# Performance work log

Hardware: AMD Instinct MI355X
Metric: run time of the kernel (lower is better)

Reference implementation:

```python
import jax, jax.numpy as jnp
import numpy as np

T, N, D = 512, 32, 1024
H, P, L = 1024, 1024, 4
STDV = 1.0 / np.sqrt(H)


def setup_inputs() -> dict:
    key = jax.random.key(0)
    ks = jax.random.split(key, 11)
    u = lambda k, shape: jax.random.uniform(k, shape, jnp.float32, -STDV, STDV)
    return {
        "x": jax.random.normal(ks[0], (T, N, D), jnp.float32),
        "h0": jax.random.normal(ks[1], (L, N, P), jnp.float32),
        "c0": jax.random.normal(ks[2], (L, N, H), jnp.float32),
        "w_ih": u(ks[3], (L, D, 4 * H)),
        "w_hh": u(ks[4], (L, P, 4 * H)),
        "b_ih": u(ks[5], (L, 4 * H)),
        "b_hh": u(ks[6], (L, 4 * H)),
        "w_ic": u(ks[7], (L, H)),
        "w_fc": u(ks[8], (L, H)),
        "w_oc": u(ks[9], (L, H)),
        "w_hm": u(ks[10], (L, H, P)),
    }


def _run_layer(x, h0, c0, wih, whh, b, wic, wfc, woc, whm):
    # x: (T, N, Din); h0: (N, P); c0: (N, H)
    def step(carry, xt):
        h, c = carry
        a = xt @ wih + h @ whh + b  # (N, 4H)
        ai, af, ag, ao = jnp.split(a, 4, axis=1)
        i = jax.nn.sigmoid(ai + c * wic)
        f = jax.nn.sigmoid(af + c * wfc)
        g = jnp.tanh(ag)
        nc = f * c + i * g
        o = jax.nn.sigmoid(ao + nc * woc)
        nh = (o * jnp.tanh(nc)) @ whm  # projection -> (N, P)
        return (nh, nc), nh

    (hT, cT), ys = jax.lax.scan(step, (h0, c0), x)
    return ys, hT, cT


def reference(x, h0, c0, w_ih, w_hh, b_ih, b_hh, w_ic, w_fc, w_oc, w_hm):
    layer_input = x
    hs, cs = [], []
    for l in range(L):
        b = b_ih[l] + b_hh[l]
        layer_input, hT, cT = _run_layer(
            layer_input, h0[l], c0[l], w_ih[l], w_hh[l], b,
            w_ic[l], w_fc[l], w_oc[l], w_hm[l])
        hs.append(hT)
        cs.append(cT)
    return layer_input, jnp.stack(hs, 0), jnp.stack(cs, 0)
```

## Files before the change

### kernel.cpp

```cpp
#include <hip/hip_runtime.h>
#include <hip/hip_bf16.h>
#include <cstdint>
#include <cstddef>


#define TT 512
#define NBATCH 32
#define HID 1024
#define G4 4096
#define KCAT 2048

typedef __attribute__((ext_vector_type(4))) float f32x4;
typedef __attribute__((ext_vector_type(8))) short bf16x8;

static __device__ __forceinline__ uint16_t f2bf(float f) {
  uint32_t u = __builtin_bit_cast(uint32_t, f);
  uint32_t lsb = (u >> 16) & 1u;
  u += 0x7fffu + lsb;
  return (uint16_t)(u >> 16);
}

static __device__ __forceinline__ f32x4 mfma16x16(bf16x8 a, bf16x8 b, f32x4 c) {
  return __builtin_amdgcn_mfma_f32_16x16x32_bf16(a, b, c, 0, 0, 0);
}

static __device__ __forceinline__ float sigm(float v) {
  return 1.f / (1.f + __expf(-v));
}
static __device__ __forceinline__ float tanh_(float v) {
  float a = fabsf(v);
  float e = __expf(-2.f * a);
  float t = (1.f - e) / (1.f + e);
  return v < 0.f ? -t : t;
}

__global__ void __launch_bounds__(256) add_bias(const float* __restrict__ a,
                                                const float* __restrict__ b,
                                                float* __restrict__ o, int n) {
  int i = blockIdx.x * 256 + threadIdx.x;
  if (i < n) o[i] = a[i] + b[i];
}

__global__ void __launch_bounds__(256) transpose_cast(const float* __restrict__ src, int lds,
                                                      uint16_t* __restrict__ dst, int ldd) {
  const int k0 = blockIdx.x * 64;
  const int n0 = blockIdx.y * 64;
  __shared__ float tile[64][65];
  const int tid = threadIdx.x;
#pragma unroll
  for (int p = 0; p < 4; ++p) {
    int kk = (tid >> 4) + 16 * p, nq = tid & 15;
    f32x4 v = *(const f32x4*)(src + (size_t)(k0 + kk) * lds + n0 + 4 * nq);
#pragma unroll
    for (int j = 0; j < 4; ++j) tile[kk][4 * nq + j] = v[j];
  }
  __syncthreads();
#pragma unroll
  for (int p = 0; p < 2; ++p) {
    int nn = (tid >> 3) + 32 * p, kq = tid & 7;
    bf16x8 o;
#pragma unroll
    for (int i = 0; i < 8; ++i) o[i] = (short)f2bf(tile[8 * kq + i][nn]);
    *(bf16x8*)(dst + (size_t)(n0 + nn) * ldd + k0 + 8 * kq) = o;
  }
}

template <bool ABF16, bool TSTORE>
__global__ void __launch_bounds__(256) gemm_k(const void* __restrict__ Aptr, int lda,
                                              const float* __restrict__ B, int ldb,
                                              void* __restrict__ outp, int ldo, int K) {
  const int m0 = blockIdx.x * 32;
  const int n0 = blockIdx.y * 64;
  __shared__ __align__(16) uint16_t As[32 * 40];
  __shared__ __align__(16) uint16_t Bs[64 * 40];
  __shared__ __align__(16) float Cs[32 * 64];
  const int tid = threadIdx.x;
  const int w = tid >> 6, lane = tid & 63;
  const int r16 = lane & 15, g = lane >> 4;

  f32x4 acc[2];
  acc[0] = (f32x4){0.f, 0.f, 0.f, 0.f};
  acc[1] = acc[0];

  for (int k0 = 0; k0 < K; k0 += 32) {
    {
      int m = tid >> 3, kq = tid & 7;
      uint16_t* d = As + m * 40 + 4 * kq;
      if (ABF16) {
        const uint16_t* A = (const uint16_t*)Aptr;
        *(uint64_t*)d = *(const uint64_t*)(A + (size_t)(m0 + m) * lda + k0 + 4 * kq);
      } else {
        const float* A = (const float*)Aptr;
        f32x4 v = *(const f32x4*)(A + (size_t)(m0 + m) * lda + k0 + 4 * kq);
        uint64_t pk = (uint64_t)f2bf(v[0]) | ((uint64_t)f2bf(v[1]) << 16) |
                      ((uint64_t)f2bf(v[2]) << 32) | ((uint64_t)f2bf(v[3]) << 48);
        *(uint64_t*)d = pk;
      }
    }
#pragma unroll
    for (int p = 0; p < 2; ++p) {
      int k = (tid >> 4) + 16 * p, nq = tid & 15;
      f32x4 v = *(const f32x4*)(B + (size_t)(k0 + k) * ldb + n0 + 4 * nq);
#pragma unroll
      for (int j = 0; j < 4; ++j) Bs[(4 * nq + j) * 40 + k] = f2bf(v[j]);
    }
    __syncthreads();
    bf16x8 a0 = *(const bf16x8*)(As + r16 * 40 + 8 * g);
    bf16x8 a1 = *(const bf16x8*)(As + (r16 + 16) * 40 + 8 * g);
    bf16x8 b = *(const bf16x8*)(Bs + (16 * w + r16) * 40 + 8 * g);
    acc[0] = mfma16x16(a0, b, acc[0]);
    acc[1] = mfma16x16(a1, b, acc[1]);
    __syncthreads();
  }

  if (TSTORE) {
#pragma unroll
    for (int rt = 0; rt < 2; ++rt)
#pragma unroll
      for (int i2 = 0; i2 < 4; ++i2)
        Cs[(16 * rt + 4 * g + i2) * 64 + 16 * w + r16] = acc[rt][i2];
    __syncthreads();
    int nn = tid >> 2, mq = tid & 3;
    bf16x8 o;
#pragma unroll
    for (int i2 = 0; i2 < 8; ++i2) o[i2] = (short)f2bf(Cs[(8 * mq + i2) * 64 + nn]);
    uint16_t* dst = (uint16_t*)outp;
    *(bf16x8*)(dst + (size_t)(n0 + nn) * ldo + m0 + 8 * mq) = o;
  } else {
    float* C = (float*)outp;
#pragma unroll
    for (int rt = 0; rt < 2; ++rt)
#pragma unroll
      for (int i2 = 0; i2 < 4; ++i2)
        C[(size_t)(m0 + 16 * rt + 4 * g + i2) * ldo + n0 + 16 * w + r16] = acc[rt][i2];
  }
}


static __device__ __forceinline__ void mfma_phase(const uint8_t* sm, const uint16_t* Wl,
                                                  int kbase, int j0, int w, int r16, int g,
                                                  f32x4 acc[2][4]) {
#pragma unroll
  for (int i = 0; i < 8; ++i) {
    const int k0 = (4 * i + w) * 32;
    const uint32_t abyte = (uint32_t)((k0 + 8 * g) * 2);
    const uint32_t swz = (uint32_t)(r16 & 7) << 4;
    uint32_t o0 = (((uint32_t)r16) << 11) + abyte;
    o0 ^= swz;
    uint32_t o1 = (((uint32_t)(r16 + 16)) << 11) + abyte;
    o1 ^= swz;
    bf16x8 a0 = *(const bf16x8*)(sm + o0);
    bf16x8 a1 = *(const bf16x8*)(sm + o1);
#pragma unroll
    for (int s = 0; s < 4; ++s) {
      const uint16_t* bp = Wl + (size_t)(s * 1024 + j0 + r16) * KCAT + (kbase + k0 + 8 * g);
      bf16x8 b = *(const bf16x8*)bp;
      acc[0][s] = mfma16x16(a0, b, acc[0][s]);
      acc[1][s] = mfma16x16(a1, b, acc[1][s]);
    }
  }
}

__global__ void __launch_bounds__(256) lstm_slot(int slot, const float* __restrict__ x,
                                                 const float* __restrict__ wic,
                                                 const float* __restrict__ wfc,
                                                 const float* __restrict__ woc,
                                                 const float* __restrict__ r0,
                                                 const float* __restrict__ bias,
                                                 float* __restrict__ cstate,
                                                 const uint16_t* __restrict__ Wcat,
                                                 uint16_t* __restrict__ ring,
                                                 uint16_t* __restrict__ m3) {
  const int blk = blockIdx.x;
  const int l = blk >> 6;
  const int slc = blk & 63;
  const int t = slot - l;
  if (t < 0 || t >= TT) return;

  __shared__ __align__(16) uint8_t sm[65536];
  const int tid = threadIdx.x;
  const int w = tid >> 6, lane = tid & 63;
  const int r16 = lane & 15, g = lane >> 4;
  const int j0 = slc * 16;

  f32x4 acc[2][4];
#pragma unroll
  for (int a = 0; a < 2; ++a)
#pragma unroll
    for (int b = 0; b < 4; ++b) acc[a][b] = (f32x4){0.f, 0.f, 0.f, 0.f};

  if (l == 0) {
    const float* src = x + (size_t)t * (NBATCH * HID);
#pragma unroll
    for (int i = 0; i < 16; ++i) {
      int cid = i * 256 + tid;
      int r = cid >> 7, c = cid & 127;
      uint32_t off = ((uint32_t)r << 11) + ((uint32_t)c << 4);
      off ^= (uint32_t)(r & 7) << 4;
      const float* s0 = src + r * HID + c * 8;
      f32x4 v0 = *(const f32x4*)(s0);
      f32x4 v1 = *(const f32x4*)(s0 + 4);
      bf16x8 pk;
      pk[0] = (short)f2bf(v0[0]); pk[1] = (short)f2bf(v0[1]);
      pk[2] = (short)f2bf(v0[2]); pk[3] = (short)f2bf(v0[3]);
      pk[4] = (short)f2bf(v1[0]); pk[5] = (short)f2bf(v1[1]);
      pk[6] = (short)f2bf(v1[2]); pk[7] = (short)f2bf(v1[3]);
      *(bf16x8*)(sm + off) = pk;
    }
  } else {
    const uint16_t* src = ring + ((size_t)(l - 1) * 2 + (t & 1)) * (NBATCH * HID);
#pragma unroll
    for (int i = 0; i < 16; ++i) {
      int cid = i * 256 + tid;
      int r = cid >> 7, c = cid & 127;
      uint32_t off = ((uint32_t)r << 11) + ((uint32_t)c << 4);
      off ^= (uint32_t)(r & 7) << 4;
      *(f32x4*)(sm + off) = *(const f32x4*)(src + r * HID + c * 8);
    }
  }
  __syncthreads();
  const uint16_t* Wl = Wcat + (size_t)l * G4 * KCAT;
  mfma_phase(sm, Wl, 0, j0, w, r16, g, acc);
  __syncthreads();

  if (t > 0) {
    const uint16_t* src = (l < 3) ? ring + ((size_t)l * 2 + ((t - 1) & 1)) * (NBATCH * HID)
                                  : m3 + (size_t)(t - 1) * (NBATCH * HID);
#pragma unroll
    for (int i = 0; i < 16; ++i) {
      int cid = i * 256 + tid;
      int r = cid >> 7, c = cid & 127;
      uint32_t off = ((uint32_t)r << 11) + ((uint32_t)c << 4);
      off ^= (uint32_t)(r & 7) << 4;
      *(f32x4*)(sm + off) = *(const f32x4*)(src + r * HID + c * 8);
    }
    __syncthreads();
    mfma_phase(sm, Wl, 1024, j0, w, r16, g, acc);
    __syncthreads();
  }

  float* red = (float*)sm;
#pragma unroll
  for (int rt = 0; rt < 2; ++rt)
#pragma unroll
    for (int s = 0; s < 4; ++s)
      *(f32x4*)(red + (size_t)(((w * 8 + rt * 4 + s) * 64 + lane) * 4)) = acc[rt][s];
  __syncthreads();

  {
    int e = tid * 2;
    int r = e >> 4;
    int jj = e & 15;
    int rt = r >> 4, reg = r & 3;
    int lanebase = ((r & 15) >> 2) * 16;
    float gate[2][4];
#pragma unroll
    for (int q = 0; q < 2; ++q) {
      int lanec = lanebase + jj + q;
#pragma unroll
      for (int s = 0; s < 4; ++s) {
        float v = 0.f;
#pragma unroll
        for (int w2 = 0; w2 < 4; ++w2) v += red[((w2 * 8 + rt * 4 + s) * 64 + lanec) * 4 + reg];
        gate[q][s] = v;
      }
    }
    const float* wicl = wic + l * HID;
    const float* wfcl = wfc + l * HID;
    const float* wocl = woc + l * HID;
    const float* bl = bias + l * G4;
    const float* r0l = r0 + ((size_t)l * NBATCH + r) * G4;
    float* cl = cstate + ((size_t)l * NBATCH + r) * HID;
    uint16_t* mout = ((l < 3) ? ring + ((size_t)l * 2 + (t & 1)) * (NBATCH * HID)
                              : m3 + (size_t)t * (NBATCH * HID)) +
                     r * HID;
    uint32_t packed = 0;
#pragma unroll
    for (int q = 0; q < 2; ++q) {
      int hj = j0 + jj + q;
      float ai = gate[q][0] + bl[hj];
      float af = gate[q][1] + bl[1024 + hj];
      float ag = gate[q][2] + bl[2048 + hj];
      float ao = gate[q][3] + bl[3072 + hj];
      if (t == 0) {
        ai += r0l[hj];
        af += r0l[1024 + hj];
        ag += r0l[2048 + hj];
        ao += r0l[3072 + hj];
      }
      float cold = cl[hj];
      float iv = sigm(ai + cold * wicl[hj]);
      float fv = sigm(af + cold * wfcl[hj]);
      float gv = tanh_(ag);
      float nc = fv * cold + iv * gv;
      float ov = sigm(ao + nc * wocl[hj]);
      float mv = ov * tanh_(nc);
      cl[hj] = nc;
      packed |= ((uint32_t)f2bf(mv)) << (16 * q);
    }
    *(uint32_t*)(mout + j0 + jj) = packed;
  }
}

extern "C" void kernel_launch(void* const* d_in, const int* in_sizes, int n_in, void* d_out,
                              int out_size, void* d_ws, size_t ws_size, hipStream_t stream) {
  (void)in_sizes; (void)n_in; (void)out_size; (void)ws_size;
  const float* x = (const float*)d_in[0];
  const float* h0 = (const float*)d_in[1];
  const float* c0 = (const float*)d_in[2];
  const float* wih = (const float*)d_in[3];
  const float* whh = (const float*)d_in[4];
  const float* bih = (const float*)d_in[5];
  const float* bhh = (const float*)d_in[6];
  const float* wic = (const float*)d_in[7];
  const float* wfc = (const float*)d_in[8];
  const float* woc = (const float*)d_in[9];
  const float* whm = (const float*)d_in[10];

  float* ys = (float*)d_out;
  float* hs = ys + (size_t)TT * NBATCH * HID;
  float* cs = hs + (size_t)4 * NBATCH * HID;

  uint8_t* ws = (uint8_t*)d_ws;
  uint16_t* Wcat = (uint16_t*)(ws);
  uint16_t* m3 = (uint16_t*)(ws + 67108864);
  uint16_t* ring = (uint16_t*)(ws + 67108864 + 33554432);
  float* r0 = (float*)(ws + 67108864 + 33554432 + 393216);
  float* bias = (float*)(ws + 67108864 + 33554432 + 393216 + 2097152);

  hipMemcpyAsync(cs, c0, (size_t)4 * NBATCH * HID * sizeof(float), hipMemcpyDeviceToDevice,
                 stream);
  add_bias<<<64, 256, 0, stream>>>(bih, bhh, bias, 4 * G4);
  transpose_cast<<<dim3(16, 64), 256, 0, stream>>>(wih, G4, Wcat, KCAT);
  for (int l = 1; l < 4; ++l)
    gemm_k<false, true><<<dim3(32, 64), 256, 0, stream>>>(
        whm + (size_t)(l - 1) * 1048576, 1024, wih + (size_t)l * 4194304, G4,
        Wcat + (size_t)l * 8388608, KCAT, 1024);
  for (int l = 0; l < 4; ++l)
    gemm_k<false, true><<<dim3(32, 64), 256, 0, stream>>>(
        whm + (size_t)l * 1048576, 1024, whh + (size_t)l * 4194304, G4,
        Wcat + (size_t)l * 8388608 + 1024, KCAT, 1024);
  for (int l = 0; l < 4; ++l)
    gemm_k<false, false><<<dim3(1, 64), 256, 0, stream>>>(
        h0 + (size_t)l * 32768, 1024, whh + (size_t)l * 4194304, G4, r0 + (size_t)l * 131072,
        G4, 1024);

  for (int s = 0; s < TT + 3; ++s)
    lstm_slot<<<256, 256, 0, stream>>>(s, x, wic, wfc, woc, r0, bias, cs, Wcat, ring, m3);

  for (int l = 0; l < 4; ++l) {
    const uint16_t* mlast =
        (l < 3) ? ring + ((size_t)l * 2 + 1) * (NBATCH * HID) : m3 + (size_t)(TT - 1) * (NBATCH * HID);
    gemm_k<true, false><<<dim3(1, 16), 256, 0, stream>>>(mlast, 1024,
                                                         whm + (size_t)l * 1048576, 1024,
                                                         hs + (size_t)l * 32768, 1024, 1024);
  }
  gemm_k<true, false><<<dim3(512, 16), 256, 0, stream>>>(m3, 1024, whm + (size_t)3 * 1048576,
                                                         1024, ys, 1024, 1024);
}
```

Baseline: 10.68 ms.

## Rewrite LSTM step kernel and weight-prep GEMMs with larger tiles and direct fragment loads

Each per-slot LSTM kernel now uses 512 threads with 8 waves splitting K. It loads activation fragments straight from global memory (pre-cast bf16 x, ring buffers) instead of staging them through a swizzled LDS tile, which removes several barriers per step. The weight-folding and output projection GEMMs are replaced by a 128x128-tiled bf16 TN GEMM that reads pre-transposed, pre-cast weights. The extra transpose and cast passes add setup work, and the step kernel's global fragment loads may be less coalesced.

After: 8.593 ms. -19.5%, faster.

```diff
diff --git a/kernel.cpp b/kernel.cpp
--- a/kernel.cpp
+++ b/kernel.cpp
@@ -24,9 +24,7 @@
   return __builtin_amdgcn_mfma_f32_16x16x32_bf16(a, b, c, 0, 0, 0);
 }
 
-static __device__ __forceinline__ float sigm(float v) {
-  return 1.f / (1.f + __expf(-v));
-}
+static __device__ __forceinline__ float sigm(float v) { return 1.f / (1.f + __expf(-v)); }
 static __device__ __forceinline__ float tanh_(float v) {
   float a = fabsf(v);
   float e = __expf(-2.f * a);
@@ -39,6 +37,21 @@
                                                 float* __restrict__ o, int n) {
   int i = blockIdx.x * 256 + threadIdx.x;
   if (i < n) o[i] = a[i] + b[i];
+}
+
+__global__ void __launch_bounds__(256) cast_bf16(const float* __restrict__ src,
+                                                 uint16_t* __restrict__ dst, int n8) {
+  int i = blockIdx.x * 256 + threadIdx.x;
+  if (i >= n8) return;
+  const float* s = src + (size_t)i * 8;
+  f32x4 v0 = *(const f32x4*)s;
+  f32x4 v1 = *(const f32x4*)(s + 4);
+  bf16x8 o;
+  o[0] = (short)f2bf(v0[0]); o[1] = (short)f2bf(v0[1]);
+  o[2] = (short)f2bf(v0[2]); o[3] = (short)f2bf(v0[3]);
+  o[4] = (short)f2bf(v1[0]); o[5] = (short)f2bf(v1[1]);
+  o[6] = (short)f2bf(v1[2]); o[7] = (short)f2bf(v1[3]);
+  *(bf16x8*)(dst + (size_t)i * 8) = o;
 }
 
 __global__ void __launch_bounds__(256) transpose_cast(const float* __restrict__ src, int lds,
@@ -65,37 +78,79 @@
   }
 }
 
-template <bool ABF16, bool TSTORE>
-__global__ void __launch_bounds__(256) gemm_k(const void* __restrict__ Aptr, int lda,
-                                              const float* __restrict__ B, int ldb,
-                                              void* __restrict__ outp, int ldo, int K) {
-  const int m0 = blockIdx.x * 32;
-  const int n0 = blockIdx.y * 64;
+template <bool OBF16>
+__global__ void __launch_bounds__(256) gemm_tn(const uint16_t* __restrict__ A, int lda, int M,
+                                               const uint16_t* __restrict__ Bt, int ldb,
+                                               void* __restrict__ Cp, int ldc, int K) {
+  const int m0 = blockIdx.x * 128, n0 = blockIdx.y * 128;
+  __shared__ __align__(16) uint16_t As[128 * 40];
+  __shared__ __align__(16) uint16_t Bs[128 * 40];
+  const int tid = threadIdx.x;
+  const int w = tid >> 6, lane = tid & 63, r16 = lane & 15, g = lane >> 4;
+  f32x4 acc[4][4];
+#pragma unroll
+  for (int a = 0; a < 4; ++a)
+#pragma unroll
+    for (int b = 0; b < 4; ++b) acc[a][b] = (f32x4){0.f, 0.f, 0.f, 0.f};
+
+  for (int k0 = 0; k0 < K; k0 += 32) {
+#pragma unroll
+    for (int q = 0; q < 2; ++q) {
+      int c = q * 256 + tid, row = c >> 2, col = (c & 3) * 8;
+      bf16x8 va = (bf16x8){0, 0, 0, 0, 0, 0, 0, 0};
+      if (m0 + row < M) va = *(const bf16x8*)(A + (size_t)(m0 + row) * lda + k0 + col);
+      *(bf16x8*)(As + row * 40 + col) = va;
+      bf16x8 vb = *(const bf16x8*)(Bt + (size_t)(n0 + row) * ldb + k0 + col);
+      *(bf16x8*)(Bs + row * 40 + col) = vb;
+    }
+    __syncthreads();
+    bf16x8 bfr[4];
+#pragma unroll
+    for (int nf = 0; nf < 4; ++nf)
+      bfr[nf] = *(const bf16x8*)(Bs + ((w >> 1) * 64 + nf * 16 + r16) * 40 + 8 * g);
+#pragma unroll
+    for (int mf = 0; mf < 4; ++mf) {
+      bf16x8 a = *(const bf16x8*)(As + ((w & 1) * 64 + mf * 16 + r16) * 40 + 8 * g);
+#pragma unroll
+      for (int nf = 0; nf < 4; ++nf) acc[mf][nf] = mfma16x16(a, bfr[nf], acc[mf][nf]);
+    }
+    __syncthreads();
+  }
+#pragma unroll
+  for (int mf = 0; mf < 4; ++mf)
+#pragma unroll
+    for (int nf = 0; nf < 4; ++nf)
+#pragma unroll
+      for (int reg = 0; reg < 4; ++reg) {
+        int row = m0 + (w & 1) * 64 + mf * 16 + (lane >> 4) * 4 + reg;
+        int col = n0 + (w >> 1) * 64 + nf * 16 + (lane & 15);
+        if (row < M) {
+          if (OBF16)
+            ((uint16_t*)Cp)[(size_t)row * ldc + col] = f2bf(acc[mf][nf][reg]);
+          else
+            ((float*)Cp)[(size_t)row * ldc + col] = acc[mf][nf][reg];
+        }
+      }
+}
+
+__global__ void __launch_bounds__(256) gemm32_f32(const float* __restrict__ A, int lda,
+                                                  const float* __restrict__ B, int ldb,
+                                                  float* __restrict__ C, int ldc, int K) {
+  const int n0 = blockIdx.x * 64;
   __shared__ __align__(16) uint16_t As[32 * 40];
   __shared__ __align__(16) uint16_t Bs[64 * 40];
-  __shared__ __align__(16) float Cs[32 * 64];
   const int tid = threadIdx.x;
-  const int w = tid >> 6, lane = tid & 63;
-  const int r16 = lane & 15, g = lane >> 4;
-
+  const int w = tid >> 6, lane = tid & 63, r16 = lane & 15, g = lane >> 4;
   f32x4 acc[2];
   acc[0] = (f32x4){0.f, 0.f, 0.f, 0.f};
   acc[1] = acc[0];
-
   for (int k0 = 0; k0 < K; k0 += 32) {
     {
       int m = tid >> 3, kq = tid & 7;
-      uint16_t* d = As + m * 40 + 4 * kq;
-      if (ABF16) {
-        const uint16_t* A = (const uint16_t*)Aptr;
-        *(uint64_t*)d = *(const uint64_t*)(A + (size_t)(m0 + m) * lda + k0 + 4 * kq);
-      } else {
-        const float* A = (const float*)Aptr;
-        f32x4 v = *(const f32x4*)(A + (size_t)(m0 + m) * lda + k0 + 4 * kq);
-        uint64_t pk = (uint64_t)f2bf(v[0]) | ((uint64_t)f2bf(v[1]) << 16) |
-                      ((uint64_t)f2bf(v[2]) << 32) | ((uint64_t)f2bf(v[3]) << 48);
-        *(uint64_t*)d = pk;
-      }
+      f32x4 v = *(const f32x4*)(A + (size_t)m * lda + k0 + 4 * kq);
+      uint64_t pk = (uint64_t)f2bf(v[0]) | ((uint64_t)f2bf(v[1]) << 16) |
+                    ((uint64_t)f2bf(v[2]) << 32) | ((uint64_t)f2bf(v[3]) << 48);
+      *(uint64_t*)(As + m * 40 + 4 * kq) = pk;
     }
 #pragma unroll
     for (int p = 0; p < 2; ++p) {
@@ -112,56 +167,14 @@
     acc[1] = mfma16x16(a1, b, acc[1]);
     __syncthreads();
   }
-
-  if (TSTORE) {
-#pragma unroll
-    for (int rt = 0; rt < 2; ++rt)
-#pragma unroll
-      for (int i2 = 0; i2 < 4; ++i2)
-        Cs[(16 * rt + 4 * g + i2) * 64 + 16 * w + r16] = acc[rt][i2];
-    __syncthreads();
-    int nn = tid >> 2, mq = tid & 3;
-    bf16x8 o;
-#pragma unroll
-    for (int i2 = 0; i2 < 8; ++i2) o[i2] = (short)f2bf(Cs[(8 * mq + i2) * 64 + nn]);
-    uint16_t* dst = (uint16_t*)outp;
-    *(bf16x8*)(dst + (size_t)(n0 + nn) * ldo + m0 + 8 * mq) = o;
-  } else {
-    float* C = (float*)outp;
-#pragma unroll
-    for (int rt = 0; rt < 2; ++rt)
-#pragma unroll
-      for (int i2 = 0; i2 < 4; ++i2)
-        C[(size_t)(m0 + 16 * rt + 4 * g + i2) * ldo + n0 + 16 * w + r16] = acc[rt][i2];
-  }
-}
-
-
-static __device__ __forceinline__ void mfma_phase(const uint8_t* sm, const uint16_t* Wl,
-                                                  int kbase, int j0, int w, int r16, int g,
-                                                  f32x4 acc[2][4]) {
-#pragma unroll
-  for (int i = 0; i < 8; ++i) {
-    const int k0 = (4 * i + w) * 32;
-    const uint32_t abyte = (uint32_t)((k0 + 8 * g) * 2);
-    const uint32_t swz = (uint32_t)(r16 & 7) << 4;
-    uint32_t o0 = (((uint32_t)r16) << 11) + abyte;
-    o0 ^= swz;
-    uint32_t o1 = (((uint32_t)(r16 + 16)) << 11) + abyte;
-    o1 ^= swz;
-    bf16x8 a0 = *(const bf16x8*)(sm + o0);
-    bf16x8 a1 = *(const bf16x8*)(sm + o1);
-#pragma unroll
-    for (int s = 0; s < 4; ++s) {
-      const uint16_t* bp = Wl + (size_t)(s * 1024 + j0 + r16) * KCAT + (kbase + k0 + 8 * g);
-      bf16x8 b = *(const bf16x8*)bp;
-      acc[0][s] = mfma16x16(a0, b, acc[0][s]);
-      acc[1][s] = mfma16x16(a1, b, acc[1][s]);
-    }
-  }
-}
-
-__global__ void __launch_bounds__(256) lstm_slot(int slot, const float* __restrict__ x,
+#pragma unroll
+  for (int rt = 0; rt < 2; ++rt)
+#pragma unroll
+    for (int reg = 0; reg < 4; ++reg)
+      C[(size_t)(16 * rt + 4 * g + reg) * ldc + n0 + 16 * w + r16] = acc[rt][reg];
+}
+
+__global__ void __launch_bounds__(512) lstm_slot(int slot, const uint16_t* __restrict__ xbf,
                                                  const float* __restrict__ wic,
                                                  const float* __restrict__ wfc,
                                                  const float* __restrict__ woc,
@@ -177,11 +190,12 @@
   const int t = slot - l;
   if (t < 0 || t >= TT) return;
 
-  __shared__ __align__(16) uint8_t sm[65536];
+  __shared__ __align__(16) float red[16384];
   const int tid = threadIdx.x;
   const int w = tid >> 6, lane = tid & 63;
   const int r16 = lane & 15, g = lane >> 4;
   const int j0 = slc * 16;
+  const uint16_t* Wl = Wcat + (size_t)l * G4 * KCAT;
 
   f32x4 acc[2][4];
 #pragma unroll
@@ -189,116 +203,86 @@
 #pragma unroll
     for (int b = 0; b < 4; ++b) acc[a][b] = (f32x4){0.f, 0.f, 0.f, 0.f};
 
-  if (l == 0) {
-    const float* src = x + (size_t)t * (NBATCH * HID);
-#pragma unroll
-    for (int i = 0; i < 16; ++i) {
-      int cid = i * 256 + tid;
-      int r = cid >> 7, c = cid & 127;
-      uint32_t off = ((uint32_t)r << 11) + ((uint32_t)c << 4);
-      off ^= (uint32_t)(r & 7) << 4;
-      const float* s0 = src + r * HID + c * 8;
-      f32x4 v0 = *(const f32x4*)(s0);
-      f32x4 v1 = *(const f32x4*)(s0 + 4);
-      bf16x8 pk;
-      pk[0] = (short)f2bf(v0[0]); pk[1] = (short)f2bf(v0[1]);
-      pk[2] = (short)f2bf(v0[2]); pk[3] = (short)f2bf(v0[3]);
-      pk[4] = (short)f2bf(v1[0]); pk[5] = (short)f2bf(v1[1]);
-      pk[6] = (short)f2bf(v1[2]); pk[7] = (short)f2bf(v1[3]);
-      *(bf16x8*)(sm + off) = pk;
-    }
-  } else {
-    const uint16_t* src = ring + ((size_t)(l - 1) * 2 + (t & 1)) * (NBATCH * HID);
-#pragma unroll
-    for (int i = 0; i < 16; ++i) {
-      int cid = i * 256 + tid;
-      int r = cid >> 7, c = cid & 127;
-      uint32_t off = ((uint32_t)r << 11) + ((uint32_t)c << 4);
-      off ^= (uint32_t)(r & 7) << 4;
-      *(f32x4*)(sm + off) = *(const f32x4*)(src + r * HID + c * 8);
-    }
-  }
+  {
+    const uint16_t* s0 = (l == 0) ? xbf + (size_t)t * (NBATCH * HID)
+                                  : ring + ((size_t)(l - 1) * 2 + (t & 1)) * (NBATCH * HID);
+#pragma unroll
+    for (int i = 0; i < 4; ++i) {
+      const int k0 = (i * 8 + w) * 32;
+      bf16x8 a0 = *(const bf16x8*)(s0 + r16 * HID + k0 + 8 * g);
+      bf16x8 a1 = *(const bf16x8*)(s0 + (r16 + 16) * HID + k0 + 8 * g);
+#pragma unroll
+      for (int s = 0; s < 4; ++s) {
+        bf16x8 b = *(const bf16x8*)(Wl + (size_t)(s * 1024 + j0 + r16) * KCAT + k0 + 8 * g);
+        acc[0][s] = mfma16x16(a0, b, acc[0][s]);
+        acc[1][s] = mfma16x16(a1, b, acc[1][s]);
+      }
+    }
+  }
+  if (t > 0) {
+    const uint16_t* s1 = (l < 3) ? ring + ((size_t)l * 2 + ((t - 1) & 1)) * (NBATCH * HID)
+                                 : m3 + (size_t)(t - 1) * (NBATCH * HID);
+#pragma unroll
+    for (int i = 0; i < 4; ++i) {
+      const int k0 = (i * 8 + w) * 32;
+      bf16x8 a0 = *(const bf16x8*)(s1 + r16 * HID + k0 + 8 * g);
+      bf16x8 a1 = *(const bf16x8*)(s1 + (r16 + 16) * HID + k0 + 8 * g);
+#pragma unroll
+      for (int s = 0; s < 4; ++s) {
+        bf16x8 b =
+            *(const bf16x8*)(Wl + (size_t)(s * 1024 + j0 + r16) * KCAT + 1024 + k0 + 8 * g);
+        acc[0][s] = mfma16x16(a0, b, acc[0][s]);
+        acc[1][s] = mfma16x16(a1, b, acc[1][s]);
+      }
+    }
+  }
+
+#pragma unroll
+  for (int rt = 0; rt < 2; ++rt)
+#pragma unroll
+    for (int s = 0; s < 4; ++s)
+      *(f32x4*)(red + (size_t)((w * 8 + rt * 4 + s) * 64 + lane) * 4) = acc[rt][s];
   __syncthreads();
-  const uint16_t* Wl = Wcat + (size_t)l * G4 * KCAT;
-  mfma_phase(sm, Wl, 0, j0, w, r16, g, acc);
-  __syncthreads();
-
-  if (t > 0) {
-    const uint16_t* src = (l < 3) ? ring + ((size_t)l * 2 + ((t - 1) & 1)) * (NBATCH * HID)
-                                  : m3 + (size_t)(t - 1) * (NBATCH * HID);
-#pragma unroll
-    for (int i = 0; i < 16; ++i) {
-      int cid = i * 256 + tid;
-      int r = cid >> 7, c = cid & 127;
-      uint32_t off = ((uint32_t)r << 11) + ((uint32_t)c << 4);
-      off ^= (uint32_t)(r & 7) << 4;
-      *(f32x4*)(sm + off) = *(const f32x4*)(src + r * HID + c * 8);
-    }
-    __syncthreads();
-    mfma_phase(sm, Wl, 1024, j0, w, r16, g, acc);
-    __syncthreads();
-  }
-
-  float* red = (float*)sm;
-#pragma unroll
-  for (int rt = 0; rt < 2; ++rt)
-#pragma unroll
-    for (int s = 0; s < 4; ++s)
-      *(f32x4*)(red + (size_t)(((w * 8 + rt * 4 + s) * 64 + lane) * 4)) = acc[rt][s];
-  __syncthreads();
 
   {
-    int e = tid * 2;
-    int r = e >> 4;
-    int jj = e & 15;
-    int rt = r >> 4, reg = r & 3;
-    int lanebase = ((r & 15) >> 2) * 16;
-    float gate[2][4];
-#pragma unroll
-    for (int q = 0; q < 2; ++q) {
-      int lanec = lanebase + jj + q;
-#pragma unroll
-      for (int s = 0; s < 4; ++s) {
-        float v = 0.f;
-#pragma unroll
-        for (int w2 = 0; w2 < 4; ++w2) v += red[((w2 * 8 + rt * 4 + s) * 64 + lanec) * 4 + reg];
-        gate[q][s] = v;
-      }
-    }
-    const float* wicl = wic + l * HID;
-    const float* wfcl = wfc + l * HID;
-    const float* wocl = woc + l * HID;
+    const int r = tid >> 4, jj = tid & 15;
+    const int rt = r >> 4, reg = r & 3;
+    const int lanec = ((r & 15) >> 2) * 16 + jj;
+    float gate[4];
+#pragma unroll
+    for (int s = 0; s < 4; ++s) {
+      float v = 0.f;
+#pragma unroll
+      for (int w2 = 0; w2 < 8; ++w2)
+        v += red[(size_t)((w2 * 8 + rt * 4 + s) * 64 + lanec) * 4 + reg];
+      gate[s] = v;
+    }
+    const int hj = j0 + jj;
     const float* bl = bias + l * G4;
-    const float* r0l = r0 + ((size_t)l * NBATCH + r) * G4;
+    float ai = gate[0] + bl[hj];
+    float af = gate[1] + bl[1024 + hj];
+    float ag = gate[2] + bl[2048 + hj];
+    float ao = gate[3] + bl[3072 + hj];
+    if (t == 0) {
+      const float* r0l = r0 + ((size_t)l * NBATCH + r) * G4;
+      ai += r0l[hj];
+      af += r0l[1024 + hj];
+      ag += r0l[2048 + hj];
+      ao += r0l[3072 + hj];
+    }
     float* cl = cstate + ((size_t)l * NBATCH + r) * HID;
+    float cold = cl[hj];
+    float iv = sigm(ai + cold * wic[l * HID + hj]);
+    float fv = sigm(af + cold * wfc[l * HID + hj]);
+    float gv = tanh_(ag);
+    float nc = fv * cold + iv * gv;
+    float ov = sigm(ao + nc * woc[l * HID + hj]);
+    float mv = ov * tanh_(nc);
+    cl[hj] = nc;
     uint16_t* mout = ((l < 3) ? ring + ((size_t)l * 2 + (t & 1)) * (NBATCH * HID)
                               : m3 + (size_t)t * (NBATCH * HID)) +
-                     r * HID;
-    uint32_t packed = 0;
-#pragma unroll
-    for (int q = 0; q < 2; ++q) {
-      int hj = j0 + jj + q;
-      float ai = gate[q][0] + bl[hj];
-      float af = gate[q][1] + bl[1024 + hj];
-      float ag = gate[q][2] + bl[2048 + hj];
-      float ao = gate[q][3] + bl[3072 + hj];
-      if (t == 0) {
-        ai += r0l[hj];
-        af += r0l[1024 + hj];
-        ag += r0l[2048 + hj];
-        ao += r0l[3072 + hj];
-      }
-      float cold = cl[hj];
-      float iv = sigm(ai + cold * wicl[hj]);
-      float fv = sigm(af + cold * wfcl[hj]);
-      float gv = tanh_(ag);
-      float nc = fv * cold + iv * gv;
-      float ov = sigm(ao + nc * wocl[hj]);
-      float mv = ov * tanh_(nc);
-      cl[hj] = nc;
-      packed |= ((uint32_t)f2bf(mv)) << (16 * q);
-    }
-    *(uint32_t*)(mout + j0 + jj) = packed;
+                     (size_t)r * HID;
+    mout[hj] = f2bf(mv);
   }
 }
 
@@ -323,38 +307,55 @@
 
   uint8_t* ws = (uint8_t*)d_ws;
   uint16_t* Wcat = (uint16_t*)(ws);
-  uint16_t* m3 = (uint16_t*)(ws + 67108864);
-  uint16_t* ring = (uint16_t*)(ws + 67108864 + 33554432);
-  float* r0 = (float*)(ws + 67108864 + 33554432 + 393216);
-  float* bias = (float*)(ws + 67108864 + 33554432 + 393216 + 2097152);
+  uint16_t* m3 = (uint16_t*)(ws + 67108864ull);
+  uint16_t* wihT = m3;
+  uint16_t* xbf = (uint16_t*)(ws + 100663296ull);
+  uint16_t* whhT = xbf;
+  uint16_t* whm_bf = (uint16_t*)(ws + 134217728ull);
+  uint16_t* whmT = (uint16_t*)(ws + 142606336ull);
+  uint16_t* ring = (uint16_t*)(ws + 150994944ull);
+  float* r0 = (float*)(ws + 151388160ull);
+  float* bias = (float*)(ws + 153485312ull);
 
   hipMemcpyAsync(cs, c0, (size_t)4 * NBATCH * HID * sizeof(float), hipMemcpyDeviceToDevice,
                  stream);
   add_bias<<<64, 256, 0, stream>>>(bih, bhh, bias, 4 * G4);
+  cast_bf16<<<2048, 256, 0, stream>>>(whm, whm_bf, 524288);
+  for (int l = 0; l < 4; ++l)
+    transpose_cast<<<dim3(16, 16), 256, 0, stream>>>(whm + (size_t)l * 1048576, 1024,
+                                                     whmT + (size_t)l * 1048576, 1024);
   transpose_cast<<<dim3(16, 64), 256, 0, stream>>>(wih, G4, Wcat, KCAT);
   for (int l = 1; l < 4; ++l)
-    gemm_k<false, true><<<dim3(32, 64), 256, 0, stream>>>(
-        whm + (size_t)(l - 1) * 1048576, 1024, wih + (size_t)l * 4194304, G4,
+    transpose_cast<<<dim3(16, 64), 256, 0, stream>>>(wih + (size_t)l * 4194304, G4,
+                                                     wihT + (size_t)(l - 1) * 4194304, 1024);
+  for (int l = 0; l < 4; ++l)
+    transpose_cast<<<dim3(16, 64), 256, 0, stream>>>(whh + (size_t)l * 4194304, G4,
+                                                     whhT + (size_t)l * 4194304, 1024);
+  for (int l = 1; l < 4; ++l)
+    gemm_tn<true><<<dim3(32, 8), 256, 0, stream>>>(
+        wihT + (size_t)(l - 1) * 4194304, 1024, 4096, whm_bf + (size_t)(l - 1) * 1048576, 1024,
         Wcat + (size_t)l * 8388608, KCAT, 1024);
   for (int l = 0; l < 4; ++l)
-    gemm_k<false, true><<<dim3(32, 64), 256, 0, stream>>>(
-        whm + (size_t)l * 1048576, 1024, whh + (size_t)l * 4194304, G4,
+    gemm_tn<true><<<dim3(32, 8), 256, 0, stream>>>(
+        whhT + (size_t)l * 4194304, 1024, 4096, whm_bf + (size_t)l * 1048576, 1024,
         Wcat + (size_t)l * 8388608 + 1024, KCAT, 1024);
   for (int l = 0; l < 4; ++l)
-    gemm_k<false, false><<<dim3(1, 64), 256, 0, stream>>>(
-        h0 + (size_t)l * 32768, 1024, whh + (size_t)l * 4194304, G4, r0 + (size_t)l * 131072,
-        G4, 1024);
+    gemm32_f32<<<64, 256, 0, stream>>>(h0 + (size_t)l * 32768, 1024,
+                                       whh + (size_t)l * 4194304, G4, r0 + (size_t)l * 131072,
+                                       G4, 1024);
+  cast_bf16<<<8192, 256, 0, stream>>>(x, xbf, 2097152);
 
   for (int s = 0; s < TT + 3; ++s)
-    lstm_slot<<<256, 256, 0, stream>>>(s, x, wic, wfc, woc, r0, bias, cs, Wcat, ring, m3);
-
+    lstm_slot<<<256, 512, 0, stream>>>(s, xbf, wic, wfc, woc, r0, bias, cs, Wcat, ring, m3);
+
+  gemm_tn<false><<<dim3(128, 8), 256, 0, stream>>>(m3, 1024, 16384,
+                                                   whmT + (size_t)3 * 1048576, 1024, ys, 1024,
+                                                   1024);
   for (int l = 0; l < 4; ++l) {
-    const uint16_t* mlast =
-        (l < 3) ? ring + ((size_t)l * 2 + 1) * (NBATCH * HID) : m3 + (size_t)(TT - 1) * (NBATCH * HID);
-    gemm_k<true, false><<<dim3(1, 16), 256, 0, stream>>>(mlast, 1024,
-                                                         whm + (size_t)l * 1048576, 1024,
-                                                         hs + (size_t)l * 32768, 1024, 1024);
-  }
-  gemm_k<true, false><<<dim3(512, 16), 256, 0, stream>>>(m3, 1024, whm + (size_t)3 * 1048576,
-                                                         1024, ys, 1024, 1024);
-}
+    const uint16_t* mlast = (l < 3) ? ring + ((size_t)l * 2 + 1) * (NBATCH * HID)
+                                    : m3 + (size_t)(TT - 1) * (NBATCH * HID);
+    gemm_tn<false><<<dim3(1, 8), 256, 0, stream>>>(mlast, 1024, 32,
+                                                   whmT + (size_t)l * 1048576, 1024,
+                                                   hs + (size_t)l * 32768, 1024, 1024);
+  }
+}
```
